# Kernel tuning notes

Hardware: AMD Instinct MI355X
Metric: run time of the kernel (lower is better)

## Reference

```python
import jax, jax.numpy as jnp
import numpy as np

N_WRD = 2000
WCODE = 3
EMB = 32
VSIZE = 7
VIEW = (16, 16)
B = 64
CSIZE = 128


def _vcode():
    # torch.meshgrid with default 'ij' indexing, cat -> (2, H*W) -> (H*W, 2)
    x = jnp.linspace(-1.0, 1.0, VIEW[0])
    y = jnp.linspace(-1.0, 1.0, VIEW[1])
    xg, yg = jnp.meshgrid(x, y, indexing='ij')
    return jnp.stack([xg.reshape(-1), yg.reshape(-1)], axis=-1)  # (V, 2)


def setup_inputs() -> dict:
    key = jax.random.key(0)
    ks = jax.random.split(key, 20)
    s = 0.02
    d = {
        'view_cell': jax.random.normal(ks[0], (B, CSIZE, VIEW[0] * VIEW[1]), jnp.float32),
        'v': jax.random.normal(ks[1], (B, VSIZE), jnp.float32),
        'w2c_w1': jax.random.normal(ks[2], (VSIZE, 512), jnp.float32) * s,
        'w2c_b1': jnp.zeros((512,), jnp.float32),
        'w2c_w2': jax.random.normal(ks[3], (512, WCODE * N_WRD), jnp.float32) * s,
        'w2c_b2': jnp.zeros((WCODE * N_WRD,), jnp.float32),
        'fc1_w': jax.random.normal(ks[4], (WCODE, 256), jnp.float32) * s,
        'fc1_b': jnp.zeros((256,), jnp.float32),
        'fc2_w': jax.random.normal(ks[5], (256, 256), jnp.float32) * s,
        'fc2_b': jnp.zeros((256,), jnp.float32),
        'fca_w': jax.random.normal(ks[6], (256, 1), jnp.float32) * s,
        'fca_b': jnp.zeros((1,), jnp.float32),
        'fce_w': jax.random.normal(ks[7], (256, EMB), jnp.float32) * s,
        'fce_b': jnp.zeros((EMB,), jnp.float32),
        'vse_w1': jax.random.normal(ks[8], (2, 128), jnp.float32) * s,
        'vse_b1': jnp.zeros((128,), jnp.float32),
        'vse_w2': jax.random.normal(ks[9], (128, EMB), jnp.float32) * s,
        'vse_b2': jnp.zeros((EMB,), jnp.float32),
    }
    return d


def reference(view_cell, v, w2c_w1, w2c_b1, w2c_w2, w2c_b2,
              fc1_w, fc1_b, fc2_w, fc2_b, fca_w, fca_b, fce_w, fce_b,
              vse_w1, vse_b1, vse_w2, vse_b2):
    b = v.shape[0]
    # w2c: v -> per-cell world codes
    h0 = jax.nn.relu(v @ w2c_w1 + w2c_b1)                     # (B, 512)
    wcode = (h0 @ w2c_w2 + w2c_b2).reshape(-1, WCODE)          # (B*N, 3)
    h = jax.nn.relu(wcode @ fc1_w + fc1_b)                     # (B*N, 256)
    h = jax.nn.relu(h @ fc2_w + fc2_b)
    activation = jax.nn.sigmoid(h @ fca_w + fca_b).reshape(b, N_WRD, 1)
    cs_emb = (h @ fce_w + fce_b).reshape(b, N_WRD, EMB)        # (B, N, E)
    # view-space embedding of the pixel grid
    vcode = _vcode()                                           # (V, 2)
    vs = jax.nn.relu(vcode @ vse_w1 + vse_b1) @ vse_w2 + vse_b2  # (V, E)
    # relation / gated softmax routing
    relation = jnp.einsum('bne,ve->bnv', cs_emb, vs)           # (B, N, V)
    route = jax.nn.softmax(relation, axis=2) * activation      # (B, N, V)
    # write: view_cell (B, C, V) @ route^T (B, V, N) -> (B, C, N)
    wrd_cell = jnp.einsum('bcv,bnv->bcn', view_cell, route)
    return wrd_cell
```

## Files before the change

### kernel.cpp

```cpp
#include <hip/hip_runtime.h>
#include <hip/hip_bf16.h>
#include <math.h>

#define NWRD 2000
#define BB 64
#define CS 128
#define VV 256

typedef __attribute__((ext_vector_type(8)))  short short8;
typedef __attribute__((ext_vector_type(16))) float f32x16;

#define WS_FC2WT 0
#define WS_WCODE (WS_FC2WT + 32768)
#define WS_VSB   (WS_WCODE + 384000)
#define WS_W2T   (WS_VSB + 4096)
#define WS_VCB   (WS_W2T + 1536000)
#define WS_FCEWT (WS_VCB + 1048576)
#define WS_H0B   (WS_FCEWT + 4096)
#define WS_FCAWB (WS_H0B + 16384)

__device__ __forceinline__ unsigned short f2bf(float x) {
    unsigned int u = __float_as_uint(x);
    u += 0x7fffu + ((u >> 16) & 1u);
    return (unsigned short)(u >> 16);
}

#define PREP_A 1024
#define PREP_B (PREP_A + 752)
#define PREP_C (PREP_B + 128)
#define PREP_D (PREP_C + 32)
#define PREP_E (PREP_D + 16)
#define PREP_N (PREP_E + 1)
__global__ __launch_bounds__(256) void kprep(
        const float* __restrict__ vc, unsigned short* __restrict__ vcb,
        const float* __restrict__ w2, unsigned short* __restrict__ w2T,
        const float* __restrict__ v, const float* __restrict__ w2c_w1,
        const float* __restrict__ w2c_b1, unsigned short* __restrict__ h0b,
        const float* __restrict__ vse_w1, const float* __restrict__ vse_b1,
        const float* __restrict__ vse_w2, const float* __restrict__ vse_b2,
        unsigned short* __restrict__ vsb,
        const float* __restrict__ fc2_w, unsigned short* __restrict__ fc2wT,
        const float* __restrict__ fce_w, unsigned short* __restrict__ fcewT,
        const float* __restrict__ fca_w, unsigned short* __restrict__ fcawB) {
    __shared__ unsigned short smem[9216];
    int bid = blockIdx.x, t = threadIdx.x;
    if (bid < PREP_A) {
        int i = (bid * 256 + t) * 8;
        float4 f0 = *(const float4*)(vc + i);
        float4 f1 = *(const float4*)(vc + i + 4);
        union { short8 v8; unsigned short u[8]; } o;
        o.u[0] = f2bf(f0.x); o.u[1] = f2bf(f0.y); o.u[2] = f2bf(f0.z); o.u[3] = f2bf(f0.w);
        o.u[4] = f2bf(f1.x); o.u[5] = f2bf(f1.y); o.u[6] = f2bf(f1.z); o.u[7] = f2bf(f1.w);
        *(short8*)(vcb + i) = o.v8;
    } else if (bid < PREP_B) {
        unsigned short (*tile)[66] = (unsigned short(*)[66])smem;
        int b2 = bid - PREP_A;
        int n0 = (b2 % 94) * 64, k0 = (b2 / 94) * 64;
        int nl = t & 63, kb = (t >> 6) * 16;
        int nc = (n0 + nl) < 6000 ? (n0 + nl) : 5999;
#pragma unroll
        for (int i = 0; i < 16; i++)
            tile[nl][kb + i] = f2bf(w2[(size_t)(k0 + kb + i)*6000 + nc]);
        __syncthreads();
        int kl = t & 63, nb = (t >> 6) * 16;
#pragma unroll
        for (int i = 0; i < 16; i++) {
            int nn = n0 + nb + i;
            if (nn < 6000) w2T[(size_t)nn*512 + k0 + kl] = tile[nb + i][kl];
        }
    } else if (bid < PREP_C) {
        int c = bid - PREP_B;
        int b = c >> 1, j = (c & 1)*256 + t;
        float s = w2c_b1[j];
#pragma unroll
        for (int k = 0; k < 7; k++) s = fmaf(v[b*7 + k], w2c_w1[k*512 + j], s);
        h0b[b*512 + j] = f2bf(fmaxf(s, 0.f));
    } else if (bid < PREP_D) {
        float* hs = (float*)smem;
        int blk = bid - PREP_C;
        int m = t & 127, half = t >> 7;
#pragma unroll
        for (int q = 0; q < 4; q++) {
            int vloc = half*4 + q;
            int vv = blk*8 + vloc;
            float x = (2.f/15.f)*(float)(vv >> 4) - 1.f;
            float y = (2.f/15.f)*(float)(vv & 15) - 1.f;
            float h = vse_b1[m] + x*vse_w1[m] + y*vse_w1[128 + m];
            hs[vloc*128 + m] = fmaxf(h, 0.f);
        }
        __syncthreads();
        int vloc = t >> 5, e = t & 31;
        float s = vse_b2[e];
        for (int mm = 0; mm < 128; mm++) s = fmaf(hs[vloc*128 + mm], vse_w2[mm*32 + e], s);
        vsb[(blk*8 + vloc)*32 + e] = f2bf(s);
    } else if (bid < PREP_E) {
        unsigned short (*tile)[72] = (unsigned short(*)[72])smem;
        int b2 = bid - PREP_D;
        int k0t = (b2 >> 2) * 64, n0t = (b2 & 3) * 64;
        int nl = t & 63, kb = (t >> 6) * 16;
#pragma unroll
        for (int i = 0; i < 16; i++)
            tile[kb + i][nl] = f2bf(fc2_w[(size_t)(k0t + kb + i)*256 + n0t + nl]);
        __syncthreads();
        int kl = t & 63, nb = (t >> 6) * 16;
#pragma unroll
        for (int i = 0; i < 16; i++)
            fc2wT[(size_t)(n0t + nb + i)*256 + k0t + kl] = tile[kl][nb + i];
    } else {
        int e = t & 31, kb = (t >> 5) * 32;
        unsigned short tmp[32];
#pragma unroll
        for (int i = 0; i < 32; i++) tmp[i] = f2bf(fce_w[(size_t)(kb + i)*32 + e]);
#pragma unroll
        for (int i = 0; i < 4; i++)
            *(short8*)(fcewT + (size_t)e*256 + kb + i*8) = *(short8*)(tmp + i*8);
#pragma unroll
        for (int i = 0; i < 32; i++)
            fcawB[(size_t)e*256 + kb + i] = (e == 0) ? f2bf(fca_w[kb + i]) : (unsigned short)0;
    }
}

__global__ __launch_bounds__(512) void k2_gemm(const unsigned short* __restrict__ h0b,
        const unsigned short* __restrict__ w2T, const float* __restrict__ b2,
        float* __restrict__ wcode) {
    int t = threadIdx.x;
    int w = t >> 6, lane = t & 63, l31 = lane & 31, h = lane >> 5;
    int mt = w & 1, nt = w >> 1;
    int n = blockIdx.x*128 + nt*32 + l31;
    int nc = n < 6000 ? n : 5999;
    f32x16 a0v, a1v;
#pragma unroll
    for (int i = 0; i < 16; i++) { a0v[i] = 0.f; a1v[i] = 0.f; }
#pragma unroll 8
    for (int ks = 0; ks < 16; ks++) {
        int k0 = ks*16 + h*8;
        short8 af0 = *(const short8*)(h0b + (mt*32 + l31)*512 + k0);
        short8 bf0 = *(const short8*)(w2T + (size_t)nc*512 + k0);
        a0v = __builtin_amdgcn_mfma_f32_32x32x16_bf16(af0, bf0, a0v, 0, 0, 0);
        short8 af1 = *(const short8*)(h0b + (mt*32 + l31)*512 + k0 + 256);
        short8 bf1 = *(const short8*)(w2T + (size_t)nc*512 + k0 + 256);
        a1v = __builtin_amdgcn_mfma_f32_32x32x16_bf16(af1, bf1, a1v, 0, 0, 0);
    }
    if (n < 6000) {
        float bias = b2[n];
#pragma unroll
        for (int i = 0; i < 16; i++) {
            int row = (i & 3) + 8*(i >> 2) + 4*h;
            wcode[(size_t)(mt*32 + row)*6000 + n] = a0v[i] + a1v[i] + bias;
        }
    }
}

#define K45_LDS 77056
__global__ __launch_bounds__(512, 4) void k45(
        const unsigned short* __restrict__ vcb,
        const float* __restrict__ wcode,
        const float* __restrict__ fc1_w, const float* __restrict__ fc1_b,
        const unsigned short* __restrict__ fc2wT, const float* __restrict__ fc2_b,
        const float* __restrict__ fca_b_p,
        const unsigned short* __restrict__ fcawB,
        const unsigned short* __restrict__ fcewT, const float* __restrict__ fce_b,
        const unsigned short* __restrict__ vsb,
        float* __restrict__ out) {
    extern __shared__ char lds[];
    unsigned short* h1b    = (unsigned short*)lds;
    unsigned short* h2b    = (unsigned short*)(lds + 33792);
    unsigned short* routeB = h2b;
    unsigned short* embL   = (unsigned short*)(lds + 67584);
    float* actL   = (float*)(lds + 72704);
    float* wcsAll = (float*)(lds + 72960);
    float* redS   = (float*)(lds + 76032);
    int t = threadIdx.x;
    int w = t >> 6, lane = t & 63, l31 = lane & 31, h = lane >> 5;
    int b = blockIdx.y;
    int n0 = blockIdx.x * 256;

    {
        const float* wb = wcode + (size_t)b*6000;
        int i0 = n0*3 + t;
        wcsAll[t] = wb[i0 < 6000 ? i0 : 5999];
        if (t < 256) {
            int i1 = n0*3 + 512 + t;
            wcsAll[512 + t] = wb[i1 < 6000 ? i1 : 5999];
        }
    }
    int jq = (t & 63) * 4;
    float4 wa  = *(const float4*)(fc1_w + jq);
    float4 wb4 = *(const float4*)(fc1_w + 256 + jq);
    float4 wc  = *(const float4*)(fc1_w + 512 + jq);
    float4 bb4 = *(const float4*)(fc1_b + jq);
    int mtA = w & 1, na = (w >> 1) * 32, nb2 = na + 128;
    float ba = fc2_b[na + l31], bbv = fc2_b[nb2 + l31];
    float be = fce_b[l31];
    float fcab = fca_b_p[0];
    int ntR = w & 1, vq = w >> 1;
    int ctE = w >> 1, ntE = w & 1;
    size_t arowE = ((size_t)(b*128 + ctE*32 + l31))*256;
    __syncthreads();

    for (int c = 0; c < 4; c++) {
        int w0 = n0 + c*64;
#pragma unroll
        for (int rr = 0; rr < 8; rr++) {
            int r = w*8 + rr;
            const float* wr = wcsAll + (c*64 + r)*3;
            float c0 = wr[0], c1 = wr[1], c2 = wr[2];
            float v0 = fmaxf(fmaf(c2, wc.x, fmaf(c1, wb4.x, fmaf(c0, wa.x, bb4.x))), 0.f);
            float v1 = fmaxf(fmaf(c2, wc.y, fmaf(c1, wb4.y, fmaf(c0, wa.y, bb4.y))), 0.f);
            float v2 = fmaxf(fmaf(c2, wc.z, fmaf(c1, wb4.z, fmaf(c0, wa.z, bb4.z))), 0.f);
            float v3 = fmaxf(fmaf(c2, wc.w, fmaf(c1, wb4.w, fmaf(c0, wa.w, bb4.w))), 0.f);
            uint2 p;
            p.x = (unsigned int)f2bf(v0) | ((unsigned int)f2bf(v1) << 16);
            p.y = (unsigned int)f2bf(v2) | ((unsigned int)f2bf(v3) << 16);
            *(uint2*)(h1b + r*264 + jq) = p;
        }
        __syncthreads();
        {
            f32x16 c0, c1;
#pragma unroll
            for (int i = 0; i < 16; i++) { c0[i] = 0.f; c1[i] = 0.f; }
#pragma unroll 4
            for (int ks = 0; ks < 16; ks++) {
                int k0 = ks*16 + h*8;
                short8 af  = *(const short8*)(h1b + (mtA*32 + l31)*264 + k0);
                short8 bfa = *(const short8*)(fc2wT + (size_t)(na  + l31)*256 + k0);
                short8 bfb = *(const short8*)(fc2wT + (size_t)(nb2 + l31)*256 + k0);
                c0 = __builtin_amdgcn_mfma_f32_32x32x16_bf16(af, bfa, c0, 0, 0, 0);
                c1 = __builtin_amdgcn_mfma_f32_32x32x16_bf16(af, bfb, c1, 0, 0, 0);
            }
#pragma unroll
            for (int i = 0; i < 16; i++) {
                int row = (i & 3) + 8*(i >> 2) + 4*h;
                h2b[(mtA*32 + row)*264 + na  + l31] = f2bf(fmaxf(c0[i] + ba, 0.f));
                h2b[(mtA*32 + row)*264 + nb2 + l31] = f2bf(fmaxf(c1[i] + bbv, 0.f));
            }
        }
        __syncthreads();
        if (w < 2) {
            f32x16 ce;
#pragma unroll
            for (int i = 0; i < 16; i++) ce[i] = 0.f;
#pragma unroll 4
            for (int ks = 0; ks < 16; ks++) {
                int k0 = ks*16 + h*8;
                short8 af = *(const short8*)(h2b + (w*32 + l31)*264 + k0);
                short8 bf = *(const short8*)(fcewT + (size_t)l31*256 + k0);
                ce = __builtin_amdgcn_mfma_f32_32x32x16_bf16(af, bf, ce, 0, 0, 0);
            }
#pragma unroll
            for (int i = 0; i < 16; i++) {
                int row = (i & 3) + 8*(i >> 2) + 4*h;
                embL[(w*32 + row)*40 + l31] = f2bf(ce[i] + be);
            }
        } else if (w < 4) {
            int m = w - 2;
            f32x16 ca;
#pragma unroll
            for (int i = 0; i < 16; i++) ca[i] = 0.f;
#pragma unroll 4
            for (int ks = 0; ks < 16; ks++) {
                int k0 = ks*16 + h*8;
                short8 af = *(const short8*)(h2b + (m*32 + l31)*264 + k0);
                short8 bf = *(const short8*)(fcawB + (size_t)l31*256 + k0);
                ca = __builtin_amdgcn_mfma_f32_32x32x16_bf16(af, bf, ca, 0, 0, 0);
            }
            if (l31 == 0) {
#pragma unroll
                for (int i = 0; i < 16; i++) {
                    int row = (i & 3) + 8*(i >> 2) + 4*h;
                    actL[m*32 + row] = 1.f / (1.f + __expf(-(ca[i] + fcab)));
                }
            }
        }
        __syncthreads();
        int nloc = ntR*32 + l31;
        f32x16 ra[2];
#pragma unroll
        for (int mt = 0; mt < 2; mt++)
#pragma unroll
            for (int i = 0; i < 16; i++) ra[mt][i] = 0.f;
#pragma unroll
        for (int s = 0; s < 2; s++) {
            short8 bfrag = *(const short8*)(embL + nloc*40 + s*16 + h*8);
#pragma unroll
            for (int mt = 0; mt < 2; mt++) {
                int vrow = (vq*2 + mt)*32 + l31;
                short8 afrag = *(const short8*)(vsb + vrow*32 + s*16 + h*8);
                ra[mt] = __builtin_amdgcn_mfma_f32_32x32x16_bf16(afrag, bfrag, ra[mt], 0, 0, 0);
            }
        }
        float sm = 0.f;
#pragma unroll
        for (int mt = 0; mt < 2; mt++)
#pragma unroll
            for (int i = 0; i < 16; i++) {
                float e = __expf(ra[mt][i]);
                ra[mt][i] = e;
                sm += e;
            }
        sm += __shfl_xor(sm, 32);
        if (lane < 32) redS[w*32 + l31] = sm;
        __syncthreads();
        sm = 0.f;
#pragma unroll
        for (int q = 0; q < 4; q++) sm += redS[(q*2 + ntR)*32 + l31];
        float scale = actL[nloc] / sm;
#pragma unroll
        for (int mt = 0; mt < 2; mt++) {
#pragma unroll
            for (int rp = 0; rp < 4; rp++) {
                int vb = (vq*2 + mt)*32 + rp*8 + h*4;
                unsigned int p0 = (unsigned int)f2bf(ra[mt][rp*4+0]*scale)
                                | ((unsigned int)f2bf(ra[mt][rp*4+1]*scale) << 16);
                unsigned int p1 = (unsigned int)f2bf(ra[mt][rp*4+2]*scale)
                                | ((unsigned int)f2bf(ra[mt][rp*4+3]*scale) << 16);
                *(uint2*)(routeB + nloc*264 + vb) = make_uint2(p0, p1);
            }
        }
        __syncthreads();
        {
            f32x16 cc;
#pragma unroll
            for (int i = 0; i < 16; i++) cc[i] = 0.f;
            const unsigned short* rrow = routeB + (ntE*32 + l31)*264;
#pragma unroll 4
            for (int ks = 0; ks < 16; ks++) {
                int k0 = ks*16 + h*8;
                short8 bf = *(const short8*)(rrow + k0);
                short8 a0 = *(const short8*)(vcb + arowE + k0);
                cc = __builtin_amdgcn_mfma_f32_32x32x16_bf16(a0, bf, cc, 0, 0, 0);
            }
            int ng = w0 + ntE*32 + l31;
            if (ng < NWRD) {
                float* ob = out + (size_t)b*128*NWRD + ng;
#pragma unroll
                for (int i = 0; i < 16; i++) {
                    int crow = (i & 3) + 8*(i >> 2) + 4*h;
                    ob[(size_t)(ctE*32 + crow)*NWRD] = cc[i];
                }
            }
        }
    }
}

extern "C" void kernel_launch(void* const* d_in, const int* in_sizes, int n_in,
                              void* d_out, int out_size, void* d_ws, size_t ws_size,
                              hipStream_t stream) {
    const float* view_cell = (const float*)d_in[0];
    const float* v       = (const float*)d_in[1];
    const float* w2c_w1  = (const float*)d_in[2];
    const float* w2c_b1  = (const float*)d_in[3];
    const float* w2c_w2  = (const float*)d_in[4];
    const float* w2c_b2  = (const float*)d_in[5];
    const float* fc1_w   = (const float*)d_in[6];
    const float* fc1_b   = (const float*)d_in[7];
    const float* fc2_w   = (const float*)d_in[8];
    const float* fc2_b   = (const float*)d_in[9];
    const float* fca_w   = (const float*)d_in[10];
    const float* fca_b   = (const float*)d_in[11];
    const float* fce_w   = (const float*)d_in[12];
    const float* fce_b   = (const float*)d_in[13];
    const float* vse_w1  = (const float*)d_in[14];
    const float* vse_b1  = (const float*)d_in[15];
    const float* vse_w2  = (const float*)d_in[16];
    const float* vse_b2  = (const float*)d_in[17];
    float* ws    = (float*)d_ws;
    unsigned short* fc2wT = (unsigned short*)(ws + WS_FC2WT);
    float* wcode = ws + WS_WCODE;
    unsigned short* vsb   = (unsigned short*)(ws + WS_VSB);
    unsigned short* w2T   = (unsigned short*)(ws + WS_W2T);
    unsigned short* vcb   = (unsigned short*)(ws + WS_VCB);
    unsigned short* fcewT = (unsigned short*)(ws + WS_FCEWT);
    unsigned short* h0b   = (unsigned short*)(ws + WS_H0B);
    unsigned short* fcawB = (unsigned short*)(ws + WS_FCAWB);
    float* out   = (float*)d_out;

    kprep<<<PREP_N, 256, 0, stream>>>(view_cell, vcb, w2c_w2, w2T,
                                      v, w2c_w1, w2c_b1, h0b,
                                      vse_w1, vse_b1, vse_w2, vse_b2, vsb,
                                      fc2_w, fc2wT, fce_w, fcewT, fca_w, fcawB);
    k2_gemm<<<47, 512, 0, stream>>>(h0b, w2T, w2c_b2, wcode);
    (void)hipFuncSetAttribute((const void*)k45,
                              hipFuncAttributeMaxDynamicSharedMemorySize, K45_LDS);
    dim3 g45(8, 64);
    k45<<<g45, 512, K45_LDS, stream>>>(vcb, wcode, fc1_w, fc1_b, fc2wT, fc2_b,
                                       fca_b, fcawB, fcewT, fce_b, vsb, out);
}
```

Baseline: 241.3 us.

## Fuse w2c GEMM into prep kernel and use packed bf16 conversion

Removes the separate w2T transpose and h0 passes and the k2_gemm launch. The first 94 prep blocks now compute h0 on the fly, stage the bf16 w2 tile in LDS and run the MFMA GEMM directly. This drops one kernel launch and the workspace round trip for the transposed weight. In exchange each of those blocks recomputes h0 for all 64 rows and does a strided read of w2. It also swaps manual f2bf rounding for the v_cvt_pk_bf16_f32 instruction in several places and reassigns the fc2 MFMA warp tiling to share the B fragment.

```diff
diff --git a/kernel.cpp b/kernel.cpp
--- a/kernel.cpp
+++ b/kernel.cpp
@@ -24,60 +24,88 @@
     u += 0x7fffu + ((u >> 16) & 1u);
     return (unsigned short)(u >> 16);
 }
-
-#define PREP_A 1024
-#define PREP_B (PREP_A + 752)
-#define PREP_C (PREP_B + 128)
-#define PREP_D (PREP_C + 32)
-#define PREP_E (PREP_D + 16)
-#define PREP_N (PREP_E + 1)
+__device__ __forceinline__ unsigned int pkbf(float lo, float hi) {
+    unsigned int r;
+    asm("v_cvt_pk_bf16_f32 %0, %1, %2" : "=v"(r) : "v"(lo), "v"(hi));
+    return r;
+}
+
+#define PR_K2  94
+#define PR_VCB (PR_K2 + 1024)
+#define PR_VSB (PR_VCB + 32)
+#define PR_FC2 (PR_VSB + 16)
+#define PREP_N (PR_FC2 + 1)
 __global__ __launch_bounds__(256) void kprep(
         const float* __restrict__ vc, unsigned short* __restrict__ vcb,
-        const float* __restrict__ w2, unsigned short* __restrict__ w2T,
-        const float* __restrict__ v, const float* __restrict__ w2c_w1,
-        const float* __restrict__ w2c_b1, unsigned short* __restrict__ h0b,
+        const float* __restrict__ w2,
+        const float* __restrict__ v, const float* __restrict__ w1,
+        const float* __restrict__ b1, const float* __restrict__ b2,
+        float* __restrict__ wcode,
         const float* __restrict__ vse_w1, const float* __restrict__ vse_b1,
         const float* __restrict__ vse_w2, const float* __restrict__ vse_b2,
         unsigned short* __restrict__ vsb,
         const float* __restrict__ fc2_w, unsigned short* __restrict__ fc2wT,
         const float* __restrict__ fce_w, unsigned short* __restrict__ fcewT,
         const float* __restrict__ fca_w, unsigned short* __restrict__ fcawB) {
-    __shared__ unsigned short smem[9216];
+    __shared__ __align__(16) unsigned short smem[9216];
     int bid = blockIdx.x, t = threadIdx.x;
-    if (bid < PREP_A) {
-        int i = (bid * 256 + t) * 8;
+    if (bid < PR_K2) {
+        unsigned short* ha = smem;
+        unsigned short* wb = smem + 4608;
+        int n0 = bid * 64;
+        int w = t >> 6, lane = t & 63, l31 = lane & 31, h = lane >> 5;
+        int mt = w & 1, nt = w >> 1;
+        int kk = t & 63, mg = t >> 6;
+        int colc = n0 + kk; if (colc > 5999) colc = 5999;
+        f32x16 acc;
+#pragma unroll
+        for (int i = 0; i < 16; i++) acc[i] = 0.f;
+        for (int p = 0; p < 8; p++) {
+            int k0 = p * 64;
+            float w1c[7];
+#pragma unroll
+            for (int q = 0; q < 7; q++) w1c[q] = w1[q*512 + k0 + kk];
+            float bbv = b1[k0 + kk];
+#pragma unroll
+            for (int mm = 0; mm < 16; mm++) {
+                int m = mg*16 + mm;
+                float s = bbv;
+#pragma unroll
+                for (int q = 0; q < 7; q++) s = fmaf(v[m*7 + q], w1c[q], s);
+                ha[m*72 + kk] = f2bf(fmaxf(s, 0.f));
+            }
+#pragma unroll
+            for (int i = 0; i < 16; i++)
+                wb[kk*72 + mg*16 + i] = f2bf(w2[(size_t)(k0 + mg*16 + i)*6000 + colc]);
+            __syncthreads();
+#pragma unroll
+            for (int ks = 0; ks < 4; ks++) {
+                short8 af = *(const short8*)(ha + (mt*32 + l31)*72 + ks*16 + h*8);
+                short8 bf = *(const short8*)(wb + (nt*32 + l31)*72 + ks*16 + h*8);
+                acc = __builtin_amdgcn_mfma_f32_32x32x16_bf16(af, bf, acc, 0, 0, 0);
+            }
+            __syncthreads();
+        }
+        int n = n0 + nt*32 + l31;
+        if (n < 6000) {
+            float bias = b2[n];
+#pragma unroll
+            for (int i = 0; i < 16; i++) {
+                int row = (i & 3) + 8*(i >> 2) + 4*h;
+                wcode[(size_t)(mt*32 + row)*6000 + n] = acc[i] + bias;
+            }
+        }
+    } else if (bid < PR_VCB) {
+        int i = ((bid - PR_K2) * 256 + t) * 8;
         float4 f0 = *(const float4*)(vc + i);
         float4 f1 = *(const float4*)(vc + i + 4);
-        union { short8 v8; unsigned short u[8]; } o;
-        o.u[0] = f2bf(f0.x); o.u[1] = f2bf(f0.y); o.u[2] = f2bf(f0.z); o.u[3] = f2bf(f0.w);
-        o.u[4] = f2bf(f1.x); o.u[5] = f2bf(f1.y); o.u[6] = f2bf(f1.z); o.u[7] = f2bf(f1.w);
+        union { short8 v8; unsigned int u[4]; } o;
+        o.u[0] = pkbf(f0.x, f0.y); o.u[1] = pkbf(f0.z, f0.w);
+        o.u[2] = pkbf(f1.x, f1.y); o.u[3] = pkbf(f1.z, f1.w);
         *(short8*)(vcb + i) = o.v8;
-    } else if (bid < PREP_B) {
-        unsigned short (*tile)[66] = (unsigned short(*)[66])smem;
-        int b2 = bid - PREP_A;
-        int n0 = (b2 % 94) * 64, k0 = (b2 / 94) * 64;
-        int nl = t & 63, kb = (t >> 6) * 16;
-        int nc = (n0 + nl) < 6000 ? (n0 + nl) : 5999;
-#pragma unroll
-        for (int i = 0; i < 16; i++)
-            tile[nl][kb + i] = f2bf(w2[(size_t)(k0 + kb + i)*6000 + nc]);
-        __syncthreads();
-        int kl = t & 63, nb = (t >> 6) * 16;
-#pragma unroll
-        for (int i = 0; i < 16; i++) {
-            int nn = n0 + nb + i;
-            if (nn < 6000) w2T[(size_t)nn*512 + k0 + kl] = tile[nb + i][kl];
-        }
-    } else if (bid < PREP_C) {
-        int c = bid - PREP_B;
-        int b = c >> 1, j = (c & 1)*256 + t;
-        float s = w2c_b1[j];
-#pragma unroll
-        for (int k = 0; k < 7; k++) s = fmaf(v[b*7 + k], w2c_w1[k*512 + j], s);
-        h0b[b*512 + j] = f2bf(fmaxf(s, 0.f));
-    } else if (bid < PREP_D) {
+    } else if (bid < PR_VSB) {
         float* hs = (float*)smem;
-        int blk = bid - PREP_C;
+        int blk = bid - PR_VCB;
         int m = t & 127, half = t >> 7;
 #pragma unroll
         for (int q = 0; q < 4; q++) {
@@ -85,18 +113,18 @@
             int vv = blk*8 + vloc;
             float x = (2.f/15.f)*(float)(vv >> 4) - 1.f;
             float y = (2.f/15.f)*(float)(vv & 15) - 1.f;
-            float h = vse_b1[m] + x*vse_w1[m] + y*vse_w1[128 + m];
-            hs[vloc*128 + m] = fmaxf(h, 0.f);
+            float hh = vse_b1[m] + x*vse_w1[m] + y*vse_w1[128 + m];
+            hs[vloc*128 + m] = fmaxf(hh, 0.f);
         }
         __syncthreads();
         int vloc = t >> 5, e = t & 31;
         float s = vse_b2[e];
         for (int mm = 0; mm < 128; mm++) s = fmaf(hs[vloc*128 + mm], vse_w2[mm*32 + e], s);
         vsb[(blk*8 + vloc)*32 + e] = f2bf(s);
-    } else if (bid < PREP_E) {
+    } else if (bid < PR_FC2) {
         unsigned short (*tile)[72] = (unsigned short(*)[72])smem;
-        int b2 = bid - PREP_D;
-        int k0t = (b2 >> 2) * 64, n0t = (b2 & 3) * 64;
+        int b2t = bid - PR_VSB;
+        int k0t = (b2t >> 2) * 64, n0t = (b2t & 3) * 64;
         int nl = t & 63, kb = (t >> 6) * 16;
 #pragma unroll
         for (int i = 0; i < 16; i++)
@@ -117,37 +145,6 @@
 #pragma unroll
         for (int i = 0; i < 32; i++)
             fcawB[(size_t)e*256 + kb + i] = (e == 0) ? f2bf(fca_w[kb + i]) : (unsigned short)0;
-    }
-}
-
-__global__ __launch_bounds__(512) void k2_gemm(const unsigned short* __restrict__ h0b,
-        const unsigned short* __restrict__ w2T, const float* __restrict__ b2,
-        float* __restrict__ wcode) {
-    int t = threadIdx.x;
-    int w = t >> 6, lane = t & 63, l31 = lane & 31, h = lane >> 5;
-    int mt = w & 1, nt = w >> 1;
-    int n = blockIdx.x*128 + nt*32 + l31;
-    int nc = n < 6000 ? n : 5999;
-    f32x16 a0v, a1v;
-#pragma unroll
-    for (int i = 0; i < 16; i++) { a0v[i] = 0.f; a1v[i] = 0.f; }
-#pragma unroll 8
-    for (int ks = 0; ks < 16; ks++) {
-        int k0 = ks*16 + h*8;
-        short8 af0 = *(const short8*)(h0b + (mt*32 + l31)*512 + k0);
-        short8 bf0 = *(const short8*)(w2T + (size_t)nc*512 + k0);
-        a0v = __builtin_amdgcn_mfma_f32_32x32x16_bf16(af0, bf0, a0v, 0, 0, 0);
-        short8 af1 = *(const short8*)(h0b + (mt*32 + l31)*512 + k0 + 256);
-        short8 bf1 = *(const short8*)(w2T + (size_t)nc*512 + k0 + 256);
-        a1v = __builtin_amdgcn_mfma_f32_32x32x16_bf16(af1, bf1, a1v, 0, 0, 0);
-    }
-    if (n < 6000) {
-        float bias = b2[n];
-#pragma unroll
-        for (int i = 0; i < 16; i++) {
-            int row = (i & 3) + 8*(i >> 2) + 4*h;
-            wcode[(size_t)(mt*32 + row)*6000 + n] = a0v[i] + a1v[i] + bias;
-        }
     }
 }
 
@@ -189,8 +186,8 @@
     float4 wb4 = *(const float4*)(fc1_w + 256 + jq);
     float4 wc  = *(const float4*)(fc1_w + 512 + jq);
     float4 bb4 = *(const float4*)(fc1_b + jq);
-    int mtA = w & 1, na = (w >> 1) * 32, nb2 = na + 128;
-    float ba = fc2_b[na + l31], bbv = fc2_b[nb2 + l31];
+    int nW = w*32 + l31;
+    float b2v = fc2_b[nW];
     float be = fce_b[l31];
     float fcab = fca_b_p[0];
     int ntR = w & 1, vq = w >> 1;
@@ -210,8 +207,8 @@
             float v2 = fmaxf(fmaf(c2, wc.z, fmaf(c1, wb4.z, fmaf(c0, wa.z, bb4.z))), 0.f);
             float v3 = fmaxf(fmaf(c2, wc.w, fmaf(c1, wb4.w, fmaf(c0, wa.w, bb4.w))), 0.f);
             uint2 p;
-            p.x = (unsigned int)f2bf(v0) | ((unsigned int)f2bf(v1) << 16);
-            p.y = (unsigned int)f2bf(v2) | ((unsigned int)f2bf(v3) << 16);
+            p.x = pkbf(v0, v1);
+            p.y = pkbf(v2, v3);
             *(uint2*)(h1b + r*264 + jq) = p;
         }
         __syncthreads();
@@ -222,17 +219,18 @@
 #pragma unroll 4
             for (int ks = 0; ks < 16; ks++) {
                 int k0 = ks*16 + h*8;
-                short8 af  = *(const short8*)(h1b + (mtA*32 + l31)*264 + k0);
-                short8 bfa = *(const short8*)(fc2wT + (size_t)(na  + l31)*256 + k0);
-                short8 bfb = *(const short8*)(fc2wT + (size_t)(nb2 + l31)*256 + k0);
-                c0 = __builtin_amdgcn_mfma_f32_32x32x16_bf16(af, bfa, c0, 0, 0, 0);
-                c1 = __builtin_amdgcn_mfma_f32_32x32x16_bf16(af, bfb, c1, 0, 0, 0);
+                short8 bf  = *(const short8*)(fc2wT + (size_t)nW*256 + k0);
+                short8 af0 = *(const short8*)(h1b + l31*264 + k0);
+                short8 af1 = *(const short8*)(h1b + (32 + l31)*264 + k0);
+                c0 = __builtin_amdgcn_mfma_f32_32x32x16_bf16(af0, bf, c0, 0, 0, 0);
+                c1 = __builtin_amdgcn_mfma_f32_32x32x16_bf16(af1, bf, c1, 0, 0, 0);
             }
 #pragma unroll
             for (int i = 0; i < 16; i++) {
                 int row = (i & 3) + 8*(i >> 2) + 4*h;
-                h2b[(mtA*32 + row)*264 + na  + l31] = f2bf(fmaxf(c0[i] + ba, 0.f));
-                h2b[(mtA*32 + row)*264 + nb2 + l31] = f2bf(fmaxf(c1[i] + bbv, 0.f));
+                unsigned int pk = pkbf(fmaxf(c0[i] + b2v, 0.f), fmaxf(c1[i] + b2v, 0.f));
+                h2b[row*264 + nW]        = (unsigned short)pk;
+                h2b[(row + 32)*264 + nW] = (unsigned short)(pk >> 16);
             }
         }
         __syncthreads();
@@ -248,9 +246,11 @@
                 ce = __builtin_amdgcn_mfma_f32_32x32x16_bf16(af, bf, ce, 0, 0, 0);
             }
 #pragma unroll
-            for (int i = 0; i < 16; i++) {
+            for (int i = 0; i < 16; i += 2) {
                 int row = (i & 3) + 8*(i >> 2) + 4*h;
-                embL[(w*32 + row)*40 + l31] = f2bf(ce[i] + be);
+                unsigned int pk = pkbf(ce[i] + be, ce[i+1] + be);
+                embL[(w*32 + row)*40 + l31]     = (unsigned short)pk;
+                embL[(w*32 + row + 1)*40 + l31] = (unsigned short)(pk >> 16);
             }
         } else if (w < 4) {
             int m = w - 2;
@@ -310,10 +310,8 @@
 #pragma unroll
             for (int rp = 0; rp < 4; rp++) {
                 int vb = (vq*2 + mt)*32 + rp*8 + h*4;
-                unsigned int p0 = (unsigned int)f2bf(ra[mt][rp*4+0]*scale)
-                                | ((unsigned int)f2bf(ra[mt][rp*4+1]*scale) << 16);
-                unsigned int p1 = (unsigned int)f2bf(ra[mt][rp*4+2]*scale)
-                                | ((unsigned int)f2bf(ra[mt][rp*4+3]*scale) << 16);
+                unsigned int p0 = pkbf(ra[mt][rp*4+0]*scale, ra[mt][rp*4+1]*scale);
+                unsigned int p1 = pkbf(ra[mt][rp*4+2]*scale, ra[mt][rp*4+3]*scale);
                 *(uint2*)(routeB + nloc*264 + vb) = make_uint2(p0, p1);
             }
         }
@@ -368,18 +366,15 @@
     unsigned short* fc2wT = (unsigned short*)(ws + WS_FC2WT);
     float* wcode = ws + WS_WCODE;
     unsigned short* vsb   = (unsigned short*)(ws + WS_VSB);
-    unsigned short* w2T   = (unsigned short*)(ws + WS_W2T);
     unsigned short* vcb   = (unsigned short*)(ws + WS_VCB);
     unsigned short* fcewT = (unsigned short*)(ws + WS_FCEWT);
-    unsigned short* h0b   = (unsigned short*)(ws + WS_H0B);
     unsigned short* fcawB = (unsigned short*)(ws + WS_FCAWB);
     float* out   = (float*)d_out;
 
-    kprep<<<PREP_N, 256, 0, stream>>>(view_cell, vcb, w2c_w2, w2T,
-                                      v, w2c_w1, w2c_b1, h0b,
+    kprep<<<PREP_N, 256, 0, stream>>>(view_cell, vcb,
+                                      w2c_w2, v, w2c_w1, w2c_b1, w2c_b2, wcode,
                                       vse_w1, vse_b1, vse_w2, vse_b2, vsb,
                                       fc2_w, fc2wT, fce_w, fcewT, fca_w, fcawB);
-    k2_gemm<<<47, 512, 0, stream>>>(h0b, w2T, w2c_b2, wcode);
     (void)hipFuncSetAttribute((const void*)k45,
                               hipFuncAttributeMaxDynamicSharedMemorySize, K45_LDS);
     dim3 g45(8, 64);
```

New measurement: 204.1 us. 1.18x faster.
